# Performance work log

Measured on AMD Instinct MI355X. Metric: run time of the kernel, lower is better.

Reference implementation:

```python
import jax, jax.numpy as jnp
import numpy as np
from jax import lax

D_MODEL = 384; EXPAND = 2; D_INNER = EXPAND * D_MODEL; D_STATE = 14; D_CONV = 4
DT_RANK = (D_MODEL + 15) // 16  # 24
DEPTH = 4; NUM_CLASSES = 3
BS = 2; T = 16; IMG = 224; PATCH = 16; PH = IMG // PATCH; NPATCH = PH * PH  # 196


def setup_inputs() -> dict:
    key = jax.random.key(0)
    ks = jax.random.split(key, 16)
    def rn(k, shape, sc=0.02):
        return jax.random.normal(k, shape, jnp.float32) * sc
    inp = {}
    inp['x'] = jax.random.normal(ks[0], (BS, T, 3, IMG, IMG), jnp.float32)
    inp['patch_w'] = rn(ks[1], (D_MODEL, 3, PATCH, PATCH))
    inp['patch_b'] = jnp.zeros((D_MODEL,), jnp.float32)
    inp['ln1_g'] = jnp.ones((DEPTH, D_MODEL), jnp.float32)
    inp['ln1_b'] = jnp.zeros((DEPTH, D_MODEL), jnp.float32)
    inp['in_w'] = rn(ks[2], (DEPTH, 2 * D_INNER, D_MODEL))
    inp['conv_w'] = rn(ks[3], (DEPTH, D_INNER, D_CONV), 0.1)
    inp['conv_b'] = jnp.zeros((DEPTH, D_INNER), jnp.float32)
    inp['xproj_w'] = rn(ks[4], (DEPTH, DT_RANK + 2 * D_STATE, D_INNER))
    inp['dt_w'] = rn(ks[5], (DEPTH, D_INNER, DT_RANK), 0.1)
    inp['dt_b'] = jnp.full((DEPTH, D_INNER), -4.6, jnp.float32)  # softplus(-4.6) ~ 0.01
    # S4D-real init: A = [1..d_state] per channel
    inp['A_log'] = jnp.log(jnp.tile(jnp.arange(1, D_STATE + 1, dtype=jnp.float32), (DEPTH, D_INNER, 1)))
    inp['Dparam'] = jnp.ones((DEPTH, D_INNER), jnp.float32)
    inp['out_w'] = rn(ks[6], (DEPTH, D_MODEL, D_INNER))
    inp['ln2_g'] = jnp.ones((DEPTH, D_MODEL), jnp.float32)
    inp['ln2_b'] = jnp.zeros((DEPTH, D_MODEL), jnp.float32)
    inp['fc1_w'] = rn(ks[7], (DEPTH, 4 * D_MODEL, D_MODEL))
    inp['fc1_b'] = jnp.zeros((DEPTH, 4 * D_MODEL), jnp.float32)
    inp['fc2_w'] = rn(ks[8], (DEPTH, D_MODEL, 4 * D_MODEL))
    inp['fc2_b'] = jnp.zeros((DEPTH, D_MODEL), jnp.float32)
    inp['head_w'] = rn(ks[9], (NUM_CLASSES, D_MODEL))
    inp['head_b'] = jnp.zeros((NUM_CLASSES,), jnp.float32)
    return inp


def _layernorm(x, g, b):
    mu = jnp.mean(x, -1, keepdims=True)
    v = jnp.mean((x - mu) ** 2, -1, keepdims=True)
    return (x - mu) * lax.rsqrt(v + 1e-5) * g + b


def _silu(x):
    return x * jax.nn.sigmoid(x)


def _mamba(u, in_w, conv_w, conv_b, xproj_w, dt_w, dt_b, A_log, Dp, out_w):
    b, L, _ = u.shape
    xz = jnp.einsum('bld,ed->ble', u, in_w)            # (b, L, 2*d_inner)
    xi, z = jnp.split(xz, 2, axis=-1)
    # causal depthwise conv1d along L
    xpad = jnp.pad(xi, ((0, 0), (D_CONV - 1, 0), (0, 0)))
    xc = conv_b + sum(conv_w[:, k] * xpad[:, k:k + L, :] for k in range(D_CONV))
    xc = _silu(xc)                                      # (b, L, d_inner)
    dbl = jnp.einsum('ble,re->blr', xc, xproj_w)
    dt = jax.nn.softplus(jnp.einsum('blr,dr->bld', dbl[..., :DT_RANK], dt_w) + dt_b)
    Bm = dbl[..., DT_RANK:DT_RANK + D_STATE]            # (b, L, n)
    Cm = dbl[..., DT_RANK + D_STATE:]                   # (b, L, n)
    A = -jnp.exp(A_log)                                 # (d_inner, n)

    def step(h, inps):
        dt_t, B_t, C_t, x_t = inps                      # (b,d),(b,n),(b,n),(b,d)
        h = jnp.exp(dt_t[..., None] * A) * h + (dt_t * x_t)[..., None] * B_t[:, None, :]
        return h, jnp.einsum('bdn,bn->bd', h, C_t)

    h0 = jnp.zeros((b, D_INNER, D_STATE), u.dtype)
    _, ys = lax.scan(step, h0, (jnp.swapaxes(dt, 0, 1), jnp.swapaxes(Bm, 0, 1),
                                jnp.swapaxes(Cm, 0, 1), jnp.swapaxes(xc, 0, 1)))
    y = jnp.swapaxes(ys, 0, 1) + Dp * xc
    y = y * _silu(z)
    return jnp.einsum('ble,de->bld', y, out_w)


def reference(x, patch_w, patch_b, ln1_g, ln1_b, in_w, conv_w, conv_b, xproj_w, dt_w,
              dt_b, A_log, Dparam, out_w, ln2_g, ln2_b, fc1_w, fc1_b, fc2_w, fc2_b,
              head_w, head_b):
    bs, t = x.shape[:2]
    N = bs * t
    # patch embed: stride==kernel conv -> unfold + matmul
    xf = x.reshape(N, 3, PH, PATCH, PH, PATCH).transpose(0, 2, 4, 1, 3, 5).reshape(N, NPATCH, 3 * PATCH * PATCH)
    emb = xf @ patch_w.reshape(D_MODEL, -1).T + patch_b  # (N, 196, d_model)
    h = emb.reshape(bs, t * NPATCH, D_MODEL)
    for i in range(DEPTH):
        h = h + _mamba(_layernorm(h, ln1_g[i], ln1_b[i]), in_w[i], conv_w[i], conv_b[i],
                       xproj_w[i], dt_w[i], dt_b[i], A_log[i], Dparam[i], out_w[i])
        m = _layernorm(h, ln2_g[i], ln2_b[i])
        m = jax.nn.gelu(m @ fc1_w[i].T + fc1_b[i], approximate=True) @ fc2_w[i].T + fc2_b[i]
        h = h + m
    h = h.reshape(bs, t, NPATCH, D_MODEL)
    pooled = h.max(axis=2)                               # pool='max' over patch dim
    return pooled @ head_w.T + head_b                    # (bs, t, num_classes)
```

## Files before the change

kernel.cpp:

```cpp
#include <hip/hip_runtime.h>
#include <hip/hip_bf16.h>
#include <math.h>

#define D_MODEL 384
#define D_INNER 768
#define D_STATE 14
#define D_CONV 4
#define DT_RANK 24
#define DEPTH 4
#define BS 2
#define LSEQ 3136
#define NROWS 6272
#define NFRAMES 32
#define NPATCH 196
#define NC 112
#define LC 28
#define GSCAN (BS*NC*D_INNER)

enum { ACT_NONE = 0, ACT_GELU = 1, ACT_SOFTPLUS = 2 };
enum { OM_F32 = 0, OM_ATOMIC = 1, OM_BF16 = 2, OM_SPLITB = 3, OM_XPROJ = 4 };

typedef unsigned short u16;
typedef __attribute__((ext_vector_type(8))) short bf16x8;
typedef __attribute__((ext_vector_type(4))) float f32x4;

__device__ __forceinline__ void cp16(const void* g, void* l) {
    __builtin_amdgcn_global_load_lds((const __attribute__((address_space(1))) char*)g,
                                     (__attribute__((address_space(3))) char*)l, 16, 0, 0);
}
__device__ __forceinline__ float bf2f(__hip_bfloat16 v) { return __bfloat162float(v); }

__device__ __forceinline__ void pow_tree(float e1, float* pw) {
    float e2 = e1 * e1, e4 = e2 * e2, e8 = e4 * e4;
    pw[0] = e1;       pw[1] = e2;       pw[2] = e2 * e1;  pw[3] = e4;
    pw[4] = e4 * e1;  pw[5] = e4 * e2;  pw[6] = e4 * pw[2]; pw[7] = e8;
    pw[8] = e8 * e1;  pw[9] = e8 * e2;  pw[10] = e8 * pw[2]; pw[11] = e8 * e4;
    pw[12] = e8 * pw[4]; pw[13] = e8 * pw[5];
}

#define CVT_N0 294912
#define CVT_N1 2359296
#define CVT_N2 1179648
#define CVT_N3 2359296
#define CVT_N4 2359296
#define CVT_TOT (CVT_N0+CVT_N1+CVT_N2+CVT_N3+CVT_N4)
__global__ __launch_bounds__(256) void cvt_weights_k(const float* __restrict__ s0,
                                                     const float* __restrict__ s1,
                                                     const float* __restrict__ s2,
                                                     const float* __restrict__ s3,
                                                     const float* __restrict__ s4,
                                                     __hip_bfloat16* __restrict__ d) {
    int i = (blockIdx.x * 256 + threadIdx.x) * 4;
    if (i >= CVT_TOT) return;
    const float* s;
    int off;
    if (i < CVT_N0) { s = s0; off = i; }
    else if (i < CVT_N0 + CVT_N1) { s = s1; off = i - CVT_N0; }
    else if (i < CVT_N0 + CVT_N1 + CVT_N2) { s = s2; off = i - CVT_N0 - CVT_N1; }
    else if (i < CVT_N0 + CVT_N1 + CVT_N2 + CVT_N3) { s = s3; off = i - CVT_N0 - CVT_N1 - CVT_N2; }
    else { s = s4; off = i - CVT_N0 - CVT_N1 - CVT_N2 - CVT_N3; }
    float4 v = *(const float4*)(s + off);
    d[i + 0] = __float2bfloat16(v.x);
    d[i + 1] = __float2bfloat16(v.y);
    d[i + 2] = __float2bfloat16(v.z);
    d[i + 3] = __float2bfloat16(v.w);
}

#define XPJ_TOT (DEPTH*128*768)
#define DTW_TOT (DEPTH*768*32)
__global__ __launch_bounds__(256) void cvt_pads_k(const float* __restrict__ xproj_w,
                                                  const float* __restrict__ dt_w,
                                                  __hip_bfloat16* __restrict__ xpj_pad,
                                                  __hip_bfloat16* __restrict__ dtw_pad) {
    int i = blockIdx.x * 256 + threadIdx.x;
    if (i < XPJ_TOT) {
        int l = i / (128 * 768), rem = i % (128 * 768);
        int n = rem / 768, k = rem % 768;
        float v = (n < 52) ? xproj_w[(size_t)l * 52 * 768 + n * 768 + k] : 0.f;
        xpj_pad[i] = __float2bfloat16(v);
    }
    if (i < DTW_TOT) {
        int l = i / (768 * 32), rem = i % (768 * 32);
        int dch = rem / 32, kk = rem % 32;
        float v = (kk < DT_RANK) ? dt_w[(size_t)l * 768 * DT_RANK + dch * DT_RANK + kk] : 0.f;
        dtw_pad[i] = __float2bfloat16(v);
    }
}

__global__ __launch_bounds__(256) void pack_patches(const float* __restrict__ x,
                                                    __hip_bfloat16* __restrict__ xf) {
    int idx4 = blockIdx.x * 256 + threadIdx.x;
    int k = (idx4 % 192) * 4;
    int row = idx4 / 192;
    int p = row % NPATCH;
    int f = row / NPATCH;
    int c = k >> 8, i = (k >> 4) & 15, j = k & 15;
    int ph = p / 14, pw = p % 14;
    float4 v = *(const float4*)(x + ((size_t)(f * 3 + c) * 224 + ph * 16 + i) * 224 + pw * 16 + j);
    __hip_bfloat16* o = xf + (size_t)row * 768 + k;
    o[0] = __float2bfloat16(v.x);
    o[1] = __float2bfloat16(v.y);
    o[2] = __float2bfloat16(v.z);
    o[3] = __float2bfloat16(v.w);
}

template <int ACT, int OM, int NX, int NY, int KSPLIT, int BK>
__global__ __launch_bounds__(256) void gemm_mfma(const u16* __restrict__ A, int lda,
                                                 const u16* __restrict__ B, int ldb,
                                                 const float* __restrict__ bias,
                                                 void* __restrict__ Cp, void* __restrict__ Cp2,
                                                 int ldc, int K) {
    constexpr int NXK = NX * KSPLIT;
    constexpr int NSUB = BK / 32;
    const int e = blockIdx.x & 7;
    const int sblk = blockIdx.x >> 3;
    const int y0 = (e * NY) >> 3;
    const int y1 = ((e + 1) * NY) >> 3;
    if (sblk >= (y1 - y0) * NXK) return;
    const int m0 = (y0 + sblk / NXK) * 128;
    const int xe = sblk % NXK;
    const int n0 = (xe % NX) * 128;
    const int kh = xe / NX;
    const int Keff = K / KSPLIT;

    __shared__ u16 As[NSUB * 4096];
    __shared__ u16 Bs[NSUB * 4096];
    const int tid = threadIdx.x;
    const int wave = tid >> 6;
    const int lane = tid & 63;
    const int quad = lane >> 4;
    const int l16 = lane & 15;
    const int wr = (wave >> 1) * 64;
    const int wc = (wave & 1) * 64;

    const int u0 = wave * 128 + lane;
    const int u1 = u0 + 64;
    const int r0 = u0 >> 2, c0 = (u0 & 3) * 8;
    const int r1 = u1 >> 2, c1 = (u1 & 3) * 8;
    const u16* ga0 = A + (size_t)(m0 + r0) * lda + kh * Keff + c0;
    const u16* ga1 = A + (size_t)(m0 + r1) * lda + kh * Keff + c1;
    const u16* gb0 = B + (size_t)(n0 + r0) * ldb + kh * Keff + c0;
    const u16* gb1 = B + (size_t)(n0 + r1) * ldb + kh * Keff + c1;
    u16* As0 = As + wave * 1024;
    u16* As1 = As0 + 512;
    u16* Bs0 = Bs + wave * 1024;
    u16* Bs1 = Bs0 + 512;

    f32x4 acc[4][4];
#pragma unroll
    for (int i = 0; i < 4; ++i)
#pragma unroll
        for (int j = 0; j < 4; ++j) acc[i][j] = (f32x4){0.f, 0.f, 0.f, 0.f};

    for (int kt = 0; kt < Keff; kt += BK) {
#pragma unroll
        for (int ss = 0; ss < NSUB; ++ss) {
            cp16(ga0 + kt + ss * 32, As0 + ss * 4096);
            cp16(ga1 + kt + ss * 32, As1 + ss * 4096);
            cp16(gb0 + kt + ss * 32, Bs0 + ss * 4096);
            cp16(gb1 + kt + ss * 32, Bs1 + ss * 4096);
        }
        __syncthreads();
#pragma unroll
        for (int ss = 0; ss < NSUB; ++ss) {
            bf16x8 af[4], bfr[4];
#pragma unroll
            for (int i = 0; i < 4; ++i)
                af[i] = *(const bf16x8*)&As[ss * 4096 + (wr + i * 16 + l16) * 32 + quad * 8];
#pragma unroll
            for (int j = 0; j < 4; ++j)
                bfr[j] = *(const bf16x8*)&Bs[ss * 4096 + (wc + j * 16 + l16) * 32 + quad * 8];
#pragma unroll
            for (int i = 0; i < 4; ++i)
#pragma unroll
                for (int j = 0; j < 4; ++j)
                    acc[i][j] = __builtin_amdgcn_mfma_f32_16x16x32_bf16(af[i], bfr[j], acc[i][j], 0, 0, 0);
        }
        __syncthreads();
    }

    float* Cf = (float*)Cp;
    __hip_bfloat16* Cb = (__hip_bfloat16*)Cp;
    __hip_bfloat16* Cb2 = (__hip_bfloat16*)Cp2;
#pragma unroll
    for (int j = 0; j < 4; ++j) {
        const int gn = n0 + wc + j * 16 + l16;
        const float bsv = (bias && kh == 0) ? bias[gn] : 0.f;
#pragma unroll
        for (int i = 0; i < 4; ++i) {
            const int gm = m0 + wr + i * 16 + quad * 4;
#pragma unroll
            for (int r = 0; r < 4; ++r) {
                float v = acc[i][j][r] + bsv;
                if (ACT == ACT_GELU) {
                    float t = 0.7978845608028654f * (v + 0.044715f * v * v * v);
                    v = 0.5f * v * (1.f + tanhf(t));
                } else if (ACT == ACT_SOFTPLUS) {
                    v = (v > 20.f) ? v : log1pf(__expf(v));
                }
                const int gr = gm + r;
                if (OM == OM_SPLITB) {
                    if (gn < D_INNER) Cb[(size_t)gr * D_INNER + gn] = __float2bfloat16(v);
                    else Cb2[(size_t)gr * D_INNER + gn - D_INNER] = __float2bfloat16(v);
                } else if (OM == OM_XPROJ) {
                    Cf[(size_t)gr * 128 + gn] = v;
                    if (gn < 32) Cb2[(size_t)gr * 32 + gn] = __float2bfloat16(v);
                } else if (OM == OM_ATOMIC) {
                    atomicAdd(&Cf[(size_t)gr * ldc + gn], v);
                } else {
                    size_t o = (size_t)gr * ldc + gn;
                    if (OM == OM_BF16) Cb[o] = __float2bfloat16(v);
                    else Cf[o] = v;
                }
            }
        }
    }
}

__global__ __launch_bounds__(256) void layernorm_k(const float* __restrict__ x,
                                                   const float* __restrict__ g,
                                                   const float* __restrict__ b,
                                                   __hip_bfloat16* __restrict__ o) {
    int wid = blockIdx.x * 4 + (threadIdx.x >> 6);
    int lane = threadIdx.x & 63;
    const float* xr = x + (size_t)wid * D_MODEL;
    float v[6];
    float s = 0.f;
#pragma unroll
    for (int i = 0; i < 6; ++i) { v[i] = xr[lane + i * 64]; s += v[i]; }
#pragma unroll
    for (int off = 1; off < 64; off <<= 1) s += __shfl_xor(s, off, 64);
    float mean = s * (1.f / 384.f);
    float q = 0.f;
#pragma unroll
    for (int i = 0; i < 6; ++i) { float t = v[i] - mean; q += t * t; }
#pragma unroll
    for (int off = 1; off < 64; off <<= 1) q += __shfl_xor(q, off, 64);
    float rs = rsqrtf(q * (1.f / 384.f) + 1e-5f);
    __hip_bfloat16* orow = o + (size_t)wid * D_MODEL;
#pragma unroll
    for (int i = 0; i < 6; ++i) {
        int d = lane + i * 64;
        orow[d] = __float2bfloat16((v[i] - mean) * rs * g[d] + b[d]);
    }
}

__global__ __launch_bounds__(256) void conv_silu_k(const __hip_bfloat16* __restrict__ xxb,
                                                   const float* __restrict__ w,
                                                   const float* __restrict__ bias,
                                                   __hip_bfloat16* __restrict__ xcb) {
    int idx4 = blockIdx.x * 256 + threadIdx.x;
    int e = (idx4 % 192) * 4;
    int row = idx4 / 192;
    int l = row % LSEQ;
    float4 bv = *(const float4*)(bias + e);
    float acc[4] = {bv.x, bv.y, bv.z, bv.w};
    float4 w0 = *(const float4*)(w + (e + 0) * 4);
    float4 w1 = *(const float4*)(w + (e + 1) * 4);
    float4 w2 = *(const float4*)(w + (e + 2) * 4);
    float4 w3 = *(const float4*)(w + (e + 3) * 4);
    const float wv[4][4] = {{w0.x, w0.y, w0.z, w0.w}, {w1.x, w1.y, w1.z, w1.w},
                            {w2.x, w2.y, w2.z, w2.w}, {w3.x, w3.y, w3.z, w3.w}};
#pragma unroll
    for (int k = 0; k < 4; ++k) {
        if (l - 3 + k >= 0) {
            const __hip_bfloat16* xp = xxb + (size_t)(row + k - 3) * D_INNER + e;
#pragma unroll
            for (int jj = 0; jj < 4; ++jj) acc[jj] += wv[jj][k] * bf2f(xp[jj]);
        }
    }
    __hip_bfloat16* o = xcb + (size_t)row * D_INNER + e;
#pragma unroll
    for (int jj = 0; jj < 4; ++jj) {
        float sg = 1.f / (1.f + __expf(-acc[jj]));
        o[jj] = __float2bfloat16(acc[jj] * sg);
    }
}

__global__ __launch_bounds__(256) void scan_stage1(const __hip_bfloat16* __restrict__ xcb,
                                                   const __hip_bfloat16* __restrict__ DTb,
                                                   const float* __restrict__ dbl,
                                                   float* __restrict__ P,
                                                   float* __restrict__ S) {
    __shared__ float sBC[LC][28];
    int g = blockIdx.x * 256 + threadIdx.x;
    int d = g % D_INNER;
    int bc = g / D_INNER;
    int c = bc % NC, b = bc / NC;
    int l0 = c * LC;
    long rowbase = (long)b * LSEQ + l0;
    for (int t = threadIdx.x; t < LC * 28; t += 256)
        sBC[t / 28][t % 28] = dbl[(rowbase + t / 28) * 128 + 24 + (t % 28)];
    __syncthreads();
    float h[D_STATE], p[D_STATE];
#pragma unroll
    for (int n = 0; n < D_STATE; ++n) { h[n] = 0.f; p[n] = 1.f; }
#pragma unroll 4
    for (int lr = 0; lr < LC; ++lr) {
        long row = rowbase + lr;
        float dtv = bf2f(DTb[row * D_INNER + d]);
        float xv = bf2f(xcb[row * D_INNER + d]);
        float u = dtv * xv;
        float pw[D_STATE];
        pow_tree(__expf(-dtv), pw);
#pragma unroll
        for (int n = 0; n < D_STATE; ++n) {
            p[n] *= pw[n];
            h[n] = pw[n] * h[n] + u * sBC[lr][n];
        }
    }
#pragma unroll
    for (int n = 0; n < D_STATE; ++n) { P[n * GSCAN + g] = p[n]; S[n * GSCAN + g] = h[n]; }
}

__global__ __launch_bounds__(256) void scan_stage2(const float* __restrict__ P,
                                                   float* __restrict__ S) {
    int g = blockIdx.x * 256 + threadIdx.x;
    int n = g / (BS * D_INNER);
    int rem = g % (BS * D_INNER);
    int b = rem / D_INNER, d = rem % D_INNER;
    const float* Pn = P + (size_t)n * GSCAN;
    float* Sn = S + (size_t)n * GSCAN;
    float h = 0.f;
    int idx = b * NC * D_INNER + d;
#pragma unroll 4
    for (int c = 0; c < NC; ++c, idx += D_INNER) {
        float pv = Pn[idx];
        float sv = Sn[idx];
        Sn[idx] = h;
        h = pv * h + sv;
    }
}

__global__ __launch_bounds__(256) void scan_stage3(const __hip_bfloat16* __restrict__ xcb,
                                                   const __hip_bfloat16* __restrict__ zb,
                                                   const __hip_bfloat16* __restrict__ DTb,
                                                   const float* __restrict__ dbl,
                                                   const float* __restrict__ Dp,
                                                   const float* __restrict__ HI,
                                                   __hip_bfloat16* __restrict__ yb) {
    __shared__ float sBC[LC][28];
    int g = blockIdx.x * 256 + threadIdx.x;
    int d = g % D_INNER;
    int bc = g / D_INNER;
    int c = bc % NC, b = bc / NC;
    int l0 = c * LC;
    long rowbase = (long)b * LSEQ + l0;
    for (int t = threadIdx.x; t < LC * 28; t += 256)
        sBC[t / 28][t % 28] = dbl[(rowbase + t / 28) * 128 + 24 + (t % 28)];
    __syncthreads();
    float h[D_STATE];
#pragma unroll
    for (int n = 0; n < D_STATE; ++n) h[n] = HI[n * GSCAN + g];
    float Dd = Dp[d];
#pragma unroll 4
    for (int lr = 0; lr < LC; ++lr) {
        long row = rowbase + lr;
        float dtv = bf2f(DTb[row * D_INNER + d]);
        float xv = bf2f(xcb[row * D_INNER + d]);
        float zv = bf2f(zb[row * D_INNER + d]);
        float u = dtv * xv;
        float pw[D_STATE];
        pow_tree(__expf(-dtv), pw);
        float acc = 0.f;
#pragma unroll
        for (int n = 0; n < D_STATE; ++n) {
            h[n] = pw[n] * h[n] + u * sBC[lr][n];
            acc += h[n] * sBC[lr][14 + n];
        }
        float yv = acc + Dd * xv;
        float sg = 1.f / (1.f + __expf(-zv));
        yb[row * D_INNER + d] = __float2bfloat16(yv * (zv * sg));
    }
}

__global__ __launch_bounds__(256) void pool_k(const float* __restrict__ h,
                                              float* __restrict__ pooled) {
    int idx = blockIdx.x * 256 + threadIdx.x;
    int d = idx % D_MODEL, f = idx / D_MODEL;
    float m = -1e30f;
    const float* hp = h + (size_t)f * NPATCH * D_MODEL + d;
    for (int p = 0; p < NPATCH; ++p) m = fmaxf(m, hp[(size_t)p * D_MODEL]);
    pooled[idx] = m;
}

__global__ __launch_bounds__(64) void head_k(const float* __restrict__ pooled,
                                             const float* __restrict__ hw,
                                             const float* __restrict__ hb,
                                             float* __restrict__ out) {
    int o = blockIdx.x;
    int f = o / 3, cls = o % 3;
    int lane = threadIdx.x;
    float s = 0.f;
    for (int d = lane; d < D_MODEL; d += 64)
        s += pooled[f * D_MODEL + d] * hw[cls * D_MODEL + d];
#pragma unroll
    for (int off = 1; off < 64; off <<= 1) s += __shfl_xor(s, off, 64);
    if (lane == 0) out[o] = s + hb[cls];
}

extern "C" void kernel_launch(void* const* d_in, const int* in_sizes, int n_in,
                              void* d_out, int out_size, void* d_ws, size_t ws_size,
                              hipStream_t stream) {
    const float* x       = (const float*)d_in[0];
    const float* patch_w = (const float*)d_in[1];
    const float* patch_b = (const float*)d_in[2];
    const float* ln1_g   = (const float*)d_in[3];
    const float* ln1_b   = (const float*)d_in[4];
    const float* in_w    = (const float*)d_in[5];
    const float* conv_w  = (const float*)d_in[6];
    const float* conv_b  = (const float*)d_in[7];
    const float* xproj_w = (const float*)d_in[8];
    const float* dt_w    = (const float*)d_in[9];
    const float* dt_b    = (const float*)d_in[10];
    const float* Dparam  = (const float*)d_in[12];
    const float* out_w   = (const float*)d_in[13];
    const float* ln2_g   = (const float*)d_in[14];
    const float* ln2_b   = (const float*)d_in[15];
    const float* fc1_w   = (const float*)d_in[16];
    const float* fc1_b   = (const float*)d_in[17];
    const float* fc2_w   = (const float*)d_in[18];
    const float* fc2_b   = (const float*)d_in[19];
    const float* head_w  = (const float*)d_in[20];
    const float* head_b  = (const float*)d_in[21];

    float* ws = (float*)d_ws;
    float* H     = ws;
    __hip_bfloat16* XZxb = (__hip_bfloat16*)(H + 2408448);
    __hip_bfloat16* XZzb = XZxb + 4816896;
    __hip_bfloat16* XCb  = XZzb + 4816896;
    float* DBL   = (float*)(XCb + 4816896);
    __hip_bfloat16* DTRAWb = (__hip_bfloat16*)(DBL + 802816);
    __hip_bfloat16* DTb  = DTRAWb + 200704;
    __hip_bfloat16* MIDb = DTb + 4816896;
    __hip_bfloat16* Ub   = MIDb + 9633792;
    __hip_bfloat16* Yb   = Ub + 2408448;
    float* P     = (float*)(Yb + 4816896);
    float* S     = P + (size_t)D_STATE * GSCAN;
    float* POOL  = S + (size_t)D_STATE * GSCAN;
    __hip_bfloat16* Wb = (__hip_bfloat16*)(POOL + 12288);
    __hip_bfloat16* Wb_patch = Wb;
    __hip_bfloat16* Wb_in    = Wb_patch + 294912;
    __hip_bfloat16* Wb_out   = Wb_in + 2359296;
    __hip_bfloat16* Wb_fc1   = Wb_out + 1179648;
    __hip_bfloat16* Wb_fc2   = Wb_fc1 + 2359296;
    __hip_bfloat16* Wb_xpj   = Wb_fc2 + 2359296;
    __hip_bfloat16* Wb_dtw   = Wb_xpj + 393216;
    __hip_bfloat16* XFb  = XZxb;

    dim3 blk(256);
    const int G12 = 8 * 7 * 12;
    const int G3  = 8 * 7 * 3;
    const int G3K2 = 8 * 7 * 3 * 2;
    const int G6 = 8 * 7 * 6;
    const int G1 = 8 * 7 * 1;

    cvt_weights_k<<<(CVT_TOT / 4 + 255) / 256, blk, 0, stream>>>(
        patch_w, in_w, out_w, fc1_w, fc2_w, Wb_patch);
    cvt_pads_k<<<(XPJ_TOT + 255) / 256, blk, 0, stream>>>(xproj_w, dt_w, Wb_xpj, Wb_dtw);

    pack_patches<<<4704, blk, 0, stream>>>(x, XFb);
    gemm_mfma<ACT_NONE, OM_F32, 3, 49, 1, 64><<<G3, blk, 0, stream>>>(
        (const u16*)XFb, 768, (const u16*)Wb_patch, 768, patch_b, H, nullptr, D_MODEL, 768);

    for (int i = 0; i < DEPTH; ++i) {
        const float* cw   = conv_w + (size_t)i * D_INNER * D_CONV;
        const float* cb   = conv_b + (size_t)i * D_INNER;
        const float* dtb  = dt_b + (size_t)i * D_INNER;
        const float* Dpar = Dparam + (size_t)i * D_INNER;

        layernorm_k<<<NROWS / 4, blk, 0, stream>>>(H, ln1_g + i * D_MODEL, ln1_b + i * D_MODEL, Ub);
        gemm_mfma<ACT_NONE, OM_SPLITB, 12, 49, 1, 64><<<G12, blk, 0, stream>>>(
            (const u16*)Ub, 384, (const u16*)(Wb_in + (size_t)i * 1536 * 384), 384,
            nullptr, XZxb, XZzb, D_INNER, 384);
        conv_silu_k<<<4704, blk, 0, stream>>>(XZxb, cw, cb, XCb);
        gemm_mfma<ACT_NONE, OM_XPROJ, 1, 49, 1, 64><<<G1, blk, 0, stream>>>(
            (const u16*)XCb, 768, (const u16*)(Wb_xpj + (size_t)i * 128 * 768), 768,
            nullptr, DBL, DTRAWb, 128, 768);
        gemm_mfma<ACT_SOFTPLUS, OM_BF16, 6, 49, 1, 32><<<G6, blk, 0, stream>>>(
            (const u16*)DTRAWb, 32, (const u16*)(Wb_dtw + (size_t)i * 768 * 32), 32,
            dtb, DTb, nullptr, D_INNER, 32);
        scan_stage1<<<GSCAN / 256, blk, 0, stream>>>(XCb, DTb, DBL, P, S);
        scan_stage2<<<(D_STATE * BS * D_INNER) / 256, blk, 0, stream>>>(P, S);
        scan_stage3<<<GSCAN / 256, blk, 0, stream>>>(XCb, XZzb, DTb, DBL, Dpar, S, Yb);
        gemm_mfma<ACT_NONE, OM_ATOMIC, 3, 49, 2, 64><<<G3K2, blk, 0, stream>>>(
            (const u16*)Yb, 768, (const u16*)(Wb_out + (size_t)i * 384 * 768), 768,
            nullptr, H, nullptr, D_MODEL, 768);

        layernorm_k<<<NROWS / 4, blk, 0, stream>>>(H, ln2_g + i * D_MODEL, ln2_b + i * D_MODEL, Ub);
        gemm_mfma<ACT_GELU, OM_BF16, 12, 49, 1, 64><<<G12, blk, 0, stream>>>(
            (const u16*)Ub, 384, (const u16*)(Wb_fc1 + (size_t)i * 1536 * 384), 384,
            fc1_b + (size_t)i * 4 * D_MODEL, MIDb, nullptr, 4 * D_MODEL, 384);
        gemm_mfma<ACT_NONE, OM_ATOMIC, 3, 49, 2, 64><<<G3K2, blk, 0, stream>>>(
            (const u16*)MIDb, 1536, (const u16*)(Wb_fc2 + (size_t)i * 384 * 1536), 1536,
            fc2_b + (size_t)i * D_MODEL, H, nullptr, D_MODEL, 1536);
    }

    pool_k<<<48, blk, 0, stream>>>(H, POOL);
    head_k<<<NFRAMES * 3, dim3(64), 0, stream>>>(POOL, head_w, head_b, (float*)d_out);
}
```

Measured before the change: 1.114 ms.

## Merge weight-conversion and pool/head kernels, vectorize conv and scan shared loads

The two weight-conversion kernels are merged into one launch, and the max-pool and classifier-head kernels are fused into a single per-frame kernel. The depthwise conv+SiLU kernel now reads and writes four bf16 values at a time with ushort4 instead of scalar accesses. Both scan stages pull B/C values out of shared memory as float4 vectors into registers. The goal is fewer kernel launches and fewer memory instructions, at the cost of some extra register pressure in the scan kernels.

```diff
diff --git a/kernel.cpp b/kernel.cpp
--- a/kernel.cpp
+++ b/kernel.cpp
@@ -29,6 +29,10 @@
                                      (__attribute__((address_space(3))) char*)l, 16, 0, 0);
 }
 __device__ __forceinline__ float bf2f(__hip_bfloat16 v) { return __bfloat162float(v); }
+__device__ __forceinline__ float us2f(unsigned short u) {
+    unsigned int w = ((unsigned int)u) << 16;
+    return __uint_as_float(w);
+}
 
 __device__ __forceinline__ void pow_tree(float e1, float* pw) {
     float e2 = e1 * e1, e4 = e2 * e2, e8 = e4 * e4;
@@ -44,46 +48,45 @@
 #define CVT_N3 2359296
 #define CVT_N4 2359296
 #define CVT_TOT (CVT_N0+CVT_N1+CVT_N2+CVT_N3+CVT_N4)
-__global__ __launch_bounds__(256) void cvt_weights_k(const float* __restrict__ s0,
-                                                     const float* __restrict__ s1,
-                                                     const float* __restrict__ s2,
-                                                     const float* __restrict__ s3,
-                                                     const float* __restrict__ s4,
-                                                     __hip_bfloat16* __restrict__ d) {
-    int i = (blockIdx.x * 256 + threadIdx.x) * 4;
-    if (i >= CVT_TOT) return;
-    const float* s;
-    int off;
-    if (i < CVT_N0) { s = s0; off = i; }
-    else if (i < CVT_N0 + CVT_N1) { s = s1; off = i - CVT_N0; }
-    else if (i < CVT_N0 + CVT_N1 + CVT_N2) { s = s2; off = i - CVT_N0 - CVT_N1; }
-    else if (i < CVT_N0 + CVT_N1 + CVT_N2 + CVT_N3) { s = s3; off = i - CVT_N0 - CVT_N1 - CVT_N2; }
-    else { s = s4; off = i - CVT_N0 - CVT_N1 - CVT_N2 - CVT_N3; }
-    float4 v = *(const float4*)(s + off);
-    d[i + 0] = __float2bfloat16(v.x);
-    d[i + 1] = __float2bfloat16(v.y);
-    d[i + 2] = __float2bfloat16(v.z);
-    d[i + 3] = __float2bfloat16(v.w);
-}
-
 #define XPJ_TOT (DEPTH*128*768)
 #define DTW_TOT (DEPTH*768*32)
-__global__ __launch_bounds__(256) void cvt_pads_k(const float* __restrict__ xproj_w,
-                                                  const float* __restrict__ dt_w,
-                                                  __hip_bfloat16* __restrict__ xpj_pad,
-                                                  __hip_bfloat16* __restrict__ dtw_pad) {
-    int i = blockIdx.x * 256 + threadIdx.x;
-    if (i < XPJ_TOT) {
-        int l = i / (128 * 768), rem = i % (128 * 768);
+__global__ __launch_bounds__(256) void cvt_all_k(const float* __restrict__ s0,
+                                                 const float* __restrict__ s1,
+                                                 const float* __restrict__ s2,
+                                                 const float* __restrict__ s3,
+                                                 const float* __restrict__ s4,
+                                                 const float* __restrict__ xproj_w,
+                                                 const float* __restrict__ dt_w,
+                                                 __hip_bfloat16* __restrict__ d,
+                                                 __hip_bfloat16* __restrict__ xpj_pad,
+                                                 __hip_bfloat16* __restrict__ dtw_pad) {
+    int t = blockIdx.x * 256 + threadIdx.x;
+    int i = t * 4;
+    if (i < CVT_TOT) {
+        const float* s;
+        int off;
+        if (i < CVT_N0) { s = s0; off = i; }
+        else if (i < CVT_N0 + CVT_N1) { s = s1; off = i - CVT_N0; }
+        else if (i < CVT_N0 + CVT_N1 + CVT_N2) { s = s2; off = i - CVT_N0 - CVT_N1; }
+        else if (i < CVT_N0 + CVT_N1 + CVT_N2 + CVT_N3) { s = s3; off = i - CVT_N0 - CVT_N1 - CVT_N2; }
+        else { s = s4; off = i - CVT_N0 - CVT_N1 - CVT_N2 - CVT_N3; }
+        float4 v = *(const float4*)(s + off);
+        d[i + 0] = __float2bfloat16(v.x);
+        d[i + 1] = __float2bfloat16(v.y);
+        d[i + 2] = __float2bfloat16(v.z);
+        d[i + 3] = __float2bfloat16(v.w);
+    }
+    if (t < XPJ_TOT) {
+        int l = t / (128 * 768), rem = t % (128 * 768);
         int n = rem / 768, k = rem % 768;
         float v = (n < 52) ? xproj_w[(size_t)l * 52 * 768 + n * 768 + k] : 0.f;
-        xpj_pad[i] = __float2bfloat16(v);
-    }
-    if (i < DTW_TOT) {
-        int l = i / (768 * 32), rem = i % (768 * 32);
+        xpj_pad[t] = __float2bfloat16(v);
+    }
+    if (t < DTW_TOT) {
+        int l = t / (768 * 32), rem = t % (768 * 32);
         int dch = rem / 32, kk = rem % 32;
         float v = (kk < DT_RANK) ? dt_w[(size_t)l * 768 * DT_RANK + dch * DT_RANK + kk] : 0.f;
-        dtw_pad[i] = __float2bfloat16(v);
+        dtw_pad[t] = __float2bfloat16(v);
     }
 }
 
@@ -264,17 +267,27 @@
 #pragma unroll
     for (int k = 0; k < 4; ++k) {
         if (l - 3 + k >= 0) {
-            const __hip_bfloat16* xp = xxb + (size_t)(row + k - 3) * D_INNER + e;
-#pragma unroll
-            for (int jj = 0; jj < 4; ++jj) acc[jj] += wv[jj][k] * bf2f(xp[jj]);
+            ushort4 xv = *(const ushort4*)(xxb + (size_t)(row + k - 3) * D_INNER + e);
+            acc[0] += wv[0][k] * us2f(xv.x);
+            acc[1] += wv[1][k] * us2f(xv.y);
+            acc[2] += wv[2][k] * us2f(xv.z);
+            acc[3] += wv[3][k] * us2f(xv.w);
         }
     }
-    __hip_bfloat16* o = xcb + (size_t)row * D_INNER + e;
-#pragma unroll
-    for (int jj = 0; jj < 4; ++jj) {
-        float sg = 1.f / (1.f + __expf(-acc[jj]));
-        o[jj] = __float2bfloat16(acc[jj] * sg);
-    }
+    ushort4 ov;
+    {
+        float sg0 = 1.f / (1.f + __expf(-acc[0]));
+        float sg1 = 1.f / (1.f + __expf(-acc[1]));
+        float sg2 = 1.f / (1.f + __expf(-acc[2]));
+        float sg3 = 1.f / (1.f + __expf(-acc[3]));
+        __hip_bfloat16 b0 = __float2bfloat16(acc[0] * sg0);
+        __hip_bfloat16 b1 = __float2bfloat16(acc[1] * sg1);
+        __hip_bfloat16 b2 = __float2bfloat16(acc[2] * sg2);
+        __hip_bfloat16 b3 = __float2bfloat16(acc[3] * sg3);
+        ov.x = *(unsigned short*)&b0; ov.y = *(unsigned short*)&b1;
+        ov.z = *(unsigned short*)&b2; ov.w = *(unsigned short*)&b3;
+    }
+    *(ushort4*)(xcb + (size_t)row * D_INNER + e) = ov;
 }
 
 __global__ __launch_bounds__(256) void scan_stage1(const __hip_bfloat16* __restrict__ xcb,
@@ -282,15 +295,15 @@
                                                    const float* __restrict__ dbl,
                                                    float* __restrict__ P,
                                                    float* __restrict__ S) {
-    __shared__ float sBC[LC][28];
+    __shared__ float sB[LC][16];
     int g = blockIdx.x * 256 + threadIdx.x;
     int d = g % D_INNER;
     int bc = g / D_INNER;
     int c = bc % NC, b = bc / NC;
     int l0 = c * LC;
     long rowbase = (long)b * LSEQ + l0;
-    for (int t = threadIdx.x; t < LC * 28; t += 256)
-        sBC[t / 28][t % 28] = dbl[(rowbase + t / 28) * 128 + 24 + (t % 28)];
+    for (int t = threadIdx.x; t < LC * 14; t += 256)
+        sB[t / 14][t % 14] = dbl[(rowbase + t / 14) * 128 + 24 + (t % 14)];
     __syncthreads();
     float h[D_STATE], p[D_STATE];
 #pragma unroll
@@ -301,12 +314,17 @@
         float dtv = bf2f(DTb[row * D_INNER + d]);
         float xv = bf2f(xcb[row * D_INNER + d]);
         float u = dtv * xv;
+        float Bv[16];
+        *(f32x4*)(Bv + 0)  = *(const f32x4*)&sB[lr][0];
+        *(f32x4*)(Bv + 4)  = *(const f32x4*)&sB[lr][4];
+        *(f32x4*)(Bv + 8)  = *(const f32x4*)&sB[lr][8];
+        *(f32x4*)(Bv + 12) = *(const f32x4*)&sB[lr][12];
         float pw[D_STATE];
         pow_tree(__expf(-dtv), pw);
 #pragma unroll
         for (int n = 0; n < D_STATE; ++n) {
             p[n] *= pw[n];
-            h[n] = pw[n] * h[n] + u * sBC[lr][n];
+            h[n] = pw[n] * h[n] + u * Bv[n];
         }
     }
 #pragma unroll
@@ -360,13 +378,17 @@
         float xv = bf2f(xcb[row * D_INNER + d]);
         float zv = bf2f(zb[row * D_INNER + d]);
         float u = dtv * xv;
+        float BC[28];
+#pragma unroll
+        for (int q = 0; q < 7; ++q)
+            *(f32x4*)(BC + q * 4) = *(const f32x4*)&sBC[lr][q * 4];
         float pw[D_STATE];
         pow_tree(__expf(-dtv), pw);
         float acc = 0.f;
 #pragma unroll
         for (int n = 0; n < D_STATE; ++n) {
-            h[n] = pw[n] * h[n] + u * sBC[lr][n];
-            acc += h[n] * sBC[lr][14 + n];
+            h[n] = pw[n] * h[n] + u * BC[n];
+            acc += h[n] * BC[14 + n];
         }
         float yv = acc + Dd * xv;
         float sg = 1.f / (1.f + __expf(-zv));
@@ -374,29 +396,29 @@
     }
 }
 
-__global__ __launch_bounds__(256) void pool_k(const float* __restrict__ h,
-                                              float* __restrict__ pooled) {
-    int idx = blockIdx.x * 256 + threadIdx.x;
-    int d = idx % D_MODEL, f = idx / D_MODEL;
-    float m = -1e30f;
-    const float* hp = h + (size_t)f * NPATCH * D_MODEL + d;
-    for (int p = 0; p < NPATCH; ++p) m = fmaxf(m, hp[(size_t)p * D_MODEL]);
-    pooled[idx] = m;
-}
-
-__global__ __launch_bounds__(64) void head_k(const float* __restrict__ pooled,
-                                             const float* __restrict__ hw,
-                                             const float* __restrict__ hb,
-                                             float* __restrict__ out) {
-    int o = blockIdx.x;
-    int f = o / 3, cls = o % 3;
-    int lane = threadIdx.x;
-    float s = 0.f;
-    for (int d = lane; d < D_MODEL; d += 64)
-        s += pooled[f * D_MODEL + d] * hw[cls * D_MODEL + d];
-#pragma unroll
-    for (int off = 1; off < 64; off <<= 1) s += __shfl_xor(s, off, 64);
-    if (lane == 0) out[o] = s + hb[cls];
+__global__ __launch_bounds__(256) void pool_head_k(const float* __restrict__ h,
+                                                   const float* __restrict__ hw,
+                                                   const float* __restrict__ hb,
+                                                   float* __restrict__ out) {
+    __shared__ float pooled[D_MODEL];
+    int f = blockIdx.x;
+    int tid = threadIdx.x;
+    const float* hp = h + (size_t)f * NPATCH * D_MODEL;
+    for (int d = tid; d < D_MODEL; d += 256) {
+        float m = -1e30f;
+        for (int p = 0; p < NPATCH; ++p) m = fmaxf(m, hp[(size_t)p * D_MODEL + d]);
+        pooled[d] = m;
+    }
+    __syncthreads();
+    int wave = tid >> 6, lane = tid & 63;
+    if (wave < 3) {
+        float s = 0.f;
+        for (int d = lane; d < D_MODEL; d += 64)
+            s += pooled[d] * hw[wave * D_MODEL + d];
+#pragma unroll
+        for (int off = 1; off < 64; off <<= 1) s += __shfl_xor(s, off, 64);
+        if (lane == 0) out[f * 3 + wave] = s + hb[wave];
+    }
 }
 
 extern "C" void kernel_launch(void* const* d_in, const int* in_sizes, int n_in,
@@ -455,9 +477,8 @@
     const int G6 = 8 * 7 * 6;
     const int G1 = 8 * 7 * 1;
 
-    cvt_weights_k<<<(CVT_TOT / 4 + 255) / 256, blk, 0, stream>>>(
-        patch_w, in_w, out_w, fc1_w, fc2_w, Wb_patch);
-    cvt_pads_k<<<(XPJ_TOT + 255) / 256, blk, 0, stream>>>(xproj_w, dt_w, Wb_xpj, Wb_dtw);
+    cvt_all_k<<<(CVT_TOT / 4 + 255) / 256, blk, 0, stream>>>(
+        patch_w, in_w, out_w, fc1_w, fc2_w, xproj_w, dt_w, Wb_patch, Wb_xpj, Wb_dtw);
 
     pack_patches<<<4704, blk, 0, stream>>>(x, XFb);
     gemm_mfma<ACT_NONE, OM_F32, 3, 49, 1, 64><<<G3, blk, 0, stream>>>(
@@ -496,6 +517,5 @@
             fc2_b + (size_t)i * D_MODEL, H, nullptr, D_MODEL, 1536);
     }
 
-    pool_k<<<48, blk, 0, stream>>>(H, POOL);
-    head_k<<<NFRAMES * 3, dim3(64), 0, stream>>>(POOL, head_w, head_b, (float*)d_out);
-}
+    pool_head_k<<<NFRAMES, blk, 0, stream>>>(H, head_w, head_b, (float*)d_out);
+}
```

Result: slower. 1.147 ms (+3.0%).
